# Kernel optimization log

Measured on AMD Instinct MI355X. Metric: run time of the kernel, lower is better.

The kernel has to match this reference:

```python
import jax, jax.numpy as jnp
import numpy as np

B, S, D = 32, 4096, 64
EPS_DIV = 1e-8
EPS_LN = 1e-5  # torch LayerNorm default


def setup_inputs() -> dict:
    key = jax.random.key(0)
    k1, k2, k3 = jax.random.split(key, 3)
    C = jax.random.normal(k1, (B, S, D), dtype=jnp.float32)
    V = jax.random.normal(k2, (B, S, D), dtype=jnp.float32)
    W = jax.random.normal(k3, (B, S, D), dtype=jnp.float32)
    time_mod = jnp.ones((1, 1, D), dtype=jnp.float32) * 0.5  # matches init: ones * 0.5
    ln_gamma = jnp.ones((D,), dtype=jnp.float32)
    ln_beta = jnp.zeros((D,), dtype=jnp.float32)
    return {"C": C, "V": V, "W": W, "time_mod": time_mod,
            "ln_gamma": ln_gamma, "ln_beta": ln_beta}


def reference(C, V, W, time_mod, ln_gamma, ln_beta):
    # Precompute elementwise quantities once (fused, no per-step kernels)
    decay = jax.nn.sigmoid(W * time_mod)        # [B,S,D]
    eC = jnp.exp(C)                             # [B,S,D]

    # scan over sequence axis; move S to the front for lax.scan
    xs = (jnp.swapaxes(decay, 0, 1),            # [S,B,D]
          jnp.swapaxes(eC, 0, 1),
          jnp.swapaxes(V, 0, 1))

    a0 = jnp.zeros((C.shape[0], 1), dtype=C.dtype)
    b0 = jnp.zeros((C.shape[0], C.shape[2]), dtype=C.dtype)

    def step(carry, x):
        a, b = carry
        d, ec, v = x                            # each [B,D]
        a = jnp.mean(d, axis=1, keepdims=True) * a + jnp.sum(ec, axis=1, keepdims=True)
        b = d * b + ec * v
        return (a, b), b / (a + EPS_DIV)

    _, ys = jax.lax.scan(step, (a0, b0), xs)    # ys: [S,B,D]
    result = jnp.swapaxes(ys, 0, 1)             # [B,S,D]

    # LayerNorm over last dim
    mu = jnp.mean(result, axis=-1, keepdims=True)
    var = jnp.var(result, axis=-1, keepdims=True)
    normed = (result - mu) * jax.lax.rsqrt(var + EPS_LN)
    return normed * ln_gamma + ln_beta
```

## Files before the change

### kernel.cpp

```cpp
#include <hip/hip_runtime.h>
#include <hip/hip_fp16.h>

constexpr int B = 32, S = 4096, D = 64;
constexpr float EPS_DIV = 1e-8f;
constexpr float EPS_LN  = 1e-5f;

constexpr int NCG = 1024;
constexpr int LG  = S / NCG;
constexpr int CPL = NCG / 64;
constexpr int BPB = NCG / 16;

struct alignas(16) H2x4 { __half2 a, b, c, d; };

__device__ __forceinline__ float sigmoid_f(float x) {
    return __builtin_amdgcn_rcpf(1.f + __expf(-x));
}

__device__ __forceinline__ void gsum2(float& x, float& y) {
#pragma unroll
    for (int m = 1; m < 16; m <<= 1) {
        x += __shfl_xor(x, m, 64);
        y += __shfl_xor(y, m, 64);
    }
}

__global__ __launch_bounds__(256) void k1h(
    const float4* __restrict__ C4, const float4* __restrict__ V4,
    const float4* __restrict__ W4, const float* __restrict__ TM,
    float2* __restrict__ MQstep,
    float*  __restrict__ Mc, float* __restrict__ Qc,
    float4* __restrict__ Pt4, float4* __restrict__ Ot4,
    H2x4*   __restrict__ dgev)
{
    __shared__ float sp[64][17];
    __shared__ float so[64][17];

    const int t = threadIdx.x;
    const int g = t >> 4;
    const int r = t & 15;
    const int G = blockIdx.x * 16 + g;
    const int b = G >> 10;
    const int c = G & (NCG - 1);
    const int c0 = (blockIdx.x & (BPB - 1)) * 16;
    const int s0 = c * LG;
    const size_t base = (size_t)(b * S + s0) * 16 + r;
    const float4 tm = reinterpret_cast<const float4*>(TM)[r];

    float M = 1.f, Q = 0.f;
    float4 P = {1.f, 1.f, 1.f, 1.f}, O = {0.f, 0.f, 0.f, 0.f};
#pragma unroll
    for (int i = 0; i < LG; ++i) {
        const size_t idx = base + (size_t)i * 16;
        const float4 w = W4[idx], cc = C4[idx], v = V4[idx];
        float4 dg, ec;
        dg.x = sigmoid_f(w.x * tm.x); dg.y = sigmoid_f(w.y * tm.y);
        dg.z = sigmoid_f(w.z * tm.z); dg.w = sigmoid_f(w.w * tm.w);
        ec.x = __expf(cc.x); ec.y = __expf(cc.y);
        ec.z = __expf(cc.z); ec.w = __expf(cc.w);
        float sd = (dg.x + dg.y) + (dg.z + dg.w);
        float se = (ec.x + ec.y) + (ec.z + ec.w);
        gsum2(sd, se);
        const float mm = sd * (1.f / 64.f);
        if (r == 0) MQstep[b * S + s0 + i] = make_float2(mm, se);
        M *= mm;
        Q  = fmaf(mm, Q, se);
        H2x4 hq;
        hq.a = __floats2half2_rn(dg.x, ec.x * v.x);
        hq.b = __floats2half2_rn(dg.y, ec.y * v.y);
        hq.c = __floats2half2_rn(dg.z, ec.z * v.z);
        hq.d = __floats2half2_rn(dg.w, ec.w * v.w);
        dgev[idx] = hq;
        const float2 f0 = __half22float2(hq.a);
        const float2 f1 = __half22float2(hq.b);
        const float2 f2 = __half22float2(hq.c);
        const float2 f3 = __half22float2(hq.d);
        P.x *= f0.x; P.y *= f1.x; P.z *= f2.x; P.w *= f3.x;
        O.x = fmaf(f0.x, O.x, f0.y);
        O.y = fmaf(f1.x, O.y, f1.y);
        O.z = fmaf(f2.x, O.z, f2.y);
        O.w = fmaf(f3.x, O.w, f3.y);
    }
    if (r == 0) { Mc[G] = M; Qc[G] = Q; }

    sp[4*r+0][g] = P.x; sp[4*r+1][g] = P.y; sp[4*r+2][g] = P.z; sp[4*r+3][g] = P.w;
    so[4*r+0][g] = O.x; so[4*r+1][g] = O.y; so[4*r+2][g] = O.z; so[4*r+3][g] = O.w;
    __syncthreads();
    const int d  = t >> 2;
    const int cq = t & 3;
    const float4 vp = make_float4(sp[d][cq*4+0], sp[d][cq*4+1],
                                  sp[d][cq*4+2], sp[d][cq*4+3]);
    const float4 vo = make_float4(so[d][cq*4+0], so[d][cq*4+1],
                                  so[d][cq*4+2], so[d][cq*4+3]);
    const size_t row4 = (size_t)(b * D + d) * (NCG / 4);
    Pt4[row4 + (c0 >> 2) + cq] = vp;
    Ot4[row4 + (c0 >> 2) + cq] = vo;
}

__global__ __launch_bounds__(256) void k2(
    const float*  __restrict__ Mc,  const float*  __restrict__ Qc,
    const float4* __restrict__ Pt4, const float4* __restrict__ Ot4,
    float4* __restrict__ aIn4,
    float4* __restrict__ bIn4)
{
    const int wq   = threadIdx.x >> 6;
    const int lane = threadIdx.x & 63;

    if (blockIdx.x < 512) {
        const int W = blockIdx.x * 4 + wq;
        const int b = W >> 6, d = W & 63;
        const size_t row4 = (size_t)(b * D + d) * (NCG / 4);
        float pj[CPL], oj[CPL];
#pragma unroll
        for (int q4 = 0; q4 < 4; ++q4) {
            const float4 pv = Pt4[row4 + lane*4 + q4];
            const float4 ov = Ot4[row4 + lane*4 + q4];
            pj[q4*4+0] = pv.x; pj[q4*4+1] = pv.y; pj[q4*4+2] = pv.z; pj[q4*4+3] = pv.w;
            oj[q4*4+0] = ov.x; oj[q4*4+1] = ov.y; oj[q4*4+2] = ov.z; oj[q4*4+3] = ov.w;
        }
        float p = 1.f, o = 0.f;
#pragma unroll
        for (int j = 0; j < CPL; ++j) { o = fmaf(pj[j], o, oj[j]); p = pj[j] * p; }
#pragma unroll
        for (int s = 1; s < 64; s <<= 1) {
            const float pp = __shfl_up(p, s, 64);
            const float oo = __shfl_up(o, s, 64);
            if (lane >= s) { o = fmaf(p, oo, o); p = p * pp; }
        }
        float oe = __shfl_up(o, 1, 64);
        if (lane == 0) oe = 0.f;
        float bv = oe;
#pragma unroll
        for (int q4 = 0; q4 < 4; ++q4) {
            float4 w;
            w.x = bv; bv = fmaf(pj[q4*4+0], bv, oj[q4*4+0]);
            w.y = bv; bv = fmaf(pj[q4*4+1], bv, oj[q4*4+1]);
            w.z = bv; bv = fmaf(pj[q4*4+2], bv, oj[q4*4+2]);
            w.w = bv; bv = fmaf(pj[q4*4+3], bv, oj[q4*4+3]);
            bIn4[row4 + lane*4 + q4] = w;
        }
    } else {
        const int v = (blockIdx.x - 512) * 4 + wq;
        if (v >= B) return;
        const float4* Mc4 = reinterpret_cast<const float4*>(Mc) + v * (NCG / 4);
        const float4* Qc4 = reinterpret_cast<const float4*>(Qc) + v * (NCG / 4);
        float mj[CPL], qj[CPL];
#pragma unroll
        for (int q4 = 0; q4 < 4; ++q4) {
            const float4 mv = Mc4[lane*4 + q4];
            const float4 qv = Qc4[lane*4 + q4];
            mj[q4*4+0] = mv.x; mj[q4*4+1] = mv.y; mj[q4*4+2] = mv.z; mj[q4*4+3] = mv.w;
            qj[q4*4+0] = qv.x; qj[q4*4+1] = qv.y; qj[q4*4+2] = qv.z; qj[q4*4+3] = qv.w;
        }
        float m = 1.f, q = 0.f;
#pragma unroll
        for (int j = 0; j < CPL; ++j) { q = fmaf(mj[j], q, qj[j]); m = mj[j] * m; }
#pragma unroll
        for (int s = 1; s < 64; s <<= 1) {
            const float mm = __shfl_up(m, s, 64);
            const float qq = __shfl_up(q, s, 64);
            if (lane >= s) { q = fmaf(m, qq, q); m = m * mm; }
        }
        float qe = __shfl_up(q, 1, 64);
        if (lane == 0) qe = 0.f;
        float a = qe;
        float4* out4 = reinterpret_cast<float4*>(aIn4) + v * (NCG / 4);
#pragma unroll
        for (int q4 = 0; q4 < 4; ++q4) {
            float4 w;
            w.x = a; a = fmaf(mj[q4*4+0], a, qj[q4*4+0]);
            w.y = a; a = fmaf(mj[q4*4+1], a, qj[q4*4+1]);
            w.z = a; a = fmaf(mj[q4*4+2], a, qj[q4*4+2]);
            w.w = a; a = fmaf(mj[q4*4+3], a, qj[q4*4+3]);
            out4[lane*4 + q4] = w;
        }
    }
}

__global__ __launch_bounds__(256) void k3h(
    const H2x4* __restrict__ dgev,
    const float* __restrict__ Gam, const float* __restrict__ Bet,
    const float2* __restrict__ MQstep,
    const float* __restrict__ aIn, const float4* __restrict__ bInT4,
    float4* __restrict__ out4)
{
    __shared__ float sb[64][17];

    const int t = threadIdx.x;
    const int b  = blockIdx.x >> 6;
    const int c0 = (blockIdx.x & (BPB - 1)) * 16;
    {
        const int d = t >> 2, cq = t & 3;
        const float4 ld = bInT4[(size_t)(b * D + d) * (NCG / 4) + (c0 >> 2) + cq];
        sb[d][cq*4+0] = ld.x; sb[d][cq*4+1] = ld.y;
        sb[d][cq*4+2] = ld.z; sb[d][cq*4+3] = ld.w;
    }
    __syncthreads();

    const int g = t >> 4;
    const int r = t & 15;
    const int c = c0 + g;
    const int s0 = c * LG;
    const size_t base = (size_t)(b * S + s0) * 16 + r;
    const float4 g4 = reinterpret_cast<const float4*>(Gam)[r];
    const float4 b4 = reinterpret_cast<const float4*>(Bet)[r];

    float a = aIn[b * NCG + c];
    float4 bv = make_float4(sb[4*r+0][g], sb[4*r+1][g],
                            sb[4*r+2][g], sb[4*r+3][g]);
#pragma unroll
    for (int i = 0; i < LG; ++i) {
        const size_t idx = base + (size_t)i * 16;
        const H2x4 hq = dgev[idx];
        const float2 f0 = __half22float2(hq.a);
        const float2 f1 = __half22float2(hq.b);
        const float2 f2 = __half22float2(hq.c);
        const float2 f3 = __half22float2(hq.d);
        const float2 mq = MQstep[b * S + s0 + i];
        a = fmaf(mq.x, a, mq.y);
        bv.x = fmaf(f0.x, bv.x, f0.y);
        bv.y = fmaf(f1.x, bv.y, f1.y);
        bv.z = fmaf(f2.x, bv.z, f2.y);
        bv.w = fmaf(f3.x, bv.w, f3.y);
        const float inva = __builtin_amdgcn_rcpf(a + EPS_DIV);
        float4 y;
        y.x = bv.x * inva; y.y = bv.y * inva;
        y.z = bv.z * inva; y.w = bv.w * inva;
        float sy = (y.x + y.y) + (y.z + y.w);
        float sq = fmaf(y.x, y.x, y.y * y.y) + fmaf(y.z, y.z, y.w * y.w);
        gsum2(sy, sq);
        const float mu  = sy * (1.f / 64.f);
        const float var = fmaf(-mu, mu, sq * (1.f / 64.f));
        const float rs  = __builtin_amdgcn_rsqf(fmaxf(var, 0.f) + EPS_LN);
        float4 o;
        o.x = fmaf((y.x - mu) * rs, g4.x, b4.x);
        o.y = fmaf((y.y - mu) * rs, g4.y, b4.y);
        o.z = fmaf((y.z - mu) * rs, g4.z, b4.z);
        o.w = fmaf((y.w - mu) * rs, g4.w, b4.w);
        out4[idx] = o;
    }
}

__global__ __launch_bounds__(64) void k_naive(
    const float* __restrict__ Cp, const float* __restrict__ Vp,
    const float* __restrict__ Wp, const float* __restrict__ TM,
    const float* __restrict__ Gam, const float* __restrict__ Bet,
    float* __restrict__ out)
{
    const int b = blockIdx.x;
    const int lane = threadIdx.x;
    const float tm = TM[lane], g = Gam[lane], bt = Bet[lane];
    float a = 0.f, bv = 0.f;
    for (int s = 0; s < S; ++s) {
        const size_t idx = ((size_t)b * S + s) * D + lane;
        const float wv = Wp[idx], cv = Cp[idx], vv = Vp[idx];
        const float dg = sigmoid_f(wv * tm);
        const float ec = __expf(cv);
        float sd = dg, se = ec;
#pragma unroll
        for (int m = 1; m < 64; m <<= 1) {
            sd += __shfl_xor(sd, m, 64);
            se += __shfl_xor(se, m, 64);
        }
        a  = fmaf(sd * (1.f / 64.f), a, se);
        bv = fmaf(dg, bv, ec * vv);
        const float y = bv * __builtin_amdgcn_rcpf(a + EPS_DIV);
        float sy = y, sq = y * y;
#pragma unroll
        for (int m = 1; m < 64; m <<= 1) {
            sy += __shfl_xor(sy, m, 64);
            sq += __shfl_xor(sq, m, 64);
        }
        const float mu  = sy * (1.f / 64.f);
        const float var = fmaf(-mu, mu, sq * (1.f / 64.f));
        const float rs  = __builtin_amdgcn_rsqf(fmaxf(var, 0.f) + EPS_LN);
        out[idx] = fmaf((y - mu) * rs, g, bt);
    }
}

extern "C" void kernel_launch(void* const* d_in, const int* in_sizes, int n_in,
                              void* d_out, int out_size, void* d_ws, size_t ws_size,
                              hipStream_t stream) {
    const float* Cp  = (const float*)d_in[0];
    const float* Vp  = (const float*)d_in[1];
    const float* Wp  = (const float*)d_in[2];
    const float* TM  = (const float*)d_in[3];
    const float* Gam = (const float*)d_in[4];
    const float* Bet = (const float*)d_in[5];
    float* out = (float*)d_out;
    float* wsf = (float*)d_ws;

    const size_t f_mq   = (size_t)B * S * 2;
    const size_t f_scG  = (size_t)B * NCG;
    const size_t f_vecG = (size_t)B * NCG * D;
    const size_t f_base = f_mq + 3 * f_scG + 3 * f_vecG;
    const size_t f_dgev = (size_t)B * S * D;
    const size_t needH  = (f_base + f_dgev) * sizeof(float);

    if (ws_size >= needH) {
        float2* MQstep = (float2*)wsf;
        float* Mc  = wsf + f_mq;
        float* Qc  = Mc + f_scG;
        float* Pt  = Qc + f_scG;
        float* Ot  = Pt + f_vecG;
        float* aIn = Ot + f_vecG;
        float* bIn = aIn + f_scG;
        H2x4* dgev = (H2x4*)(wsf + f_base);

        const dim3 blk(256);
        const dim3 grd(B * NCG / 16);

        k1h<<<grd, blk, 0, stream>>>((const float4*)Cp, (const float4*)Vp,
                                     (const float4*)Wp, TM, MQstep, Mc, Qc,
                                     (float4*)Pt, (float4*)Ot, dgev);
        k2<<<dim3(512 + 8), blk, 0, stream>>>(Mc, Qc, (const float4*)Pt,
                                              (const float4*)Ot,
                                              (float4*)aIn, (float4*)bIn);
        k3h<<<grd, blk, 0, stream>>>(dgev, Gam, Bet, MQstep,
                                     aIn, (const float4*)bIn, (float4*)out);
        return;
    }

    k_naive<<<dim3(B), dim3(64), 0, stream>>>(Cp, Vp, Wp, TM, Gam, Bet, out);
}
```

Before: 49.01 us.

## Halve chunk count, pack chunk P/O summaries as half2, nontemporal output stores

Reduces the number of sequence chunks per batch from 1024 to 512, so each chunk covers 8 steps and the cross-chunk scan works on fewer elements. Chunk decay-product and offset summaries are stored interleaved as half2 pairs instead of two fp32 arrays, which cuts intermediate traffic between the first and second kernels. The final LayerNorm output uses nontemporal stores. Storing the product and offset in half precision risks accuracy loss, especially underflow of the decay products over longer chunks, and each thread in the first and third kernels now does more serial work.

New measurement: 42.05 us. -14.2%, faster.

```diff
diff --git a/kernel.cpp b/kernel.cpp
--- a/kernel.cpp
+++ b/kernel.cpp
@@ -5,12 +5,19 @@
 constexpr float EPS_DIV = 1e-8f;
 constexpr float EPS_LN  = 1e-5f;
 
-constexpr int NCG = 1024;
+constexpr int NCG = 512;
 constexpr int LG  = S / NCG;
 constexpr int CPL = NCG / 64;
 constexpr int BPB = NCG / 16;
 
 struct alignas(16) H2x4 { __half2 a, b, c, d; };
+
+typedef float f4v __attribute__((ext_vector_type(4)));
+
+__device__ __forceinline__ void nt_store_f4(float4 v, float4* p) {
+    f4v t = {v.x, v.y, v.z, v.w};
+    __builtin_nontemporal_store(t, (f4v*)p);
+}
 
 __device__ __forceinline__ float sigmoid_f(float x) {
     return __builtin_amdgcn_rcpf(1.f + __expf(-x));
@@ -29,7 +36,7 @@
     const float4* __restrict__ W4, const float* __restrict__ TM,
     float2* __restrict__ MQstep,
     float*  __restrict__ Mc, float* __restrict__ Qc,
-    float4* __restrict__ Pt4, float4* __restrict__ Ot4,
+    H2x4*   __restrict__ POt,
     H2x4*   __restrict__ dgev)
 {
     __shared__ float sp[64][17];
@@ -39,7 +46,7 @@
     const int g = t >> 4;
     const int r = t & 15;
     const int G = blockIdx.x * 16 + g;
-    const int b = G >> 10;
+    const int b = G >> 9;
     const int c = G & (NCG - 1);
     const int c0 = (blockIdx.x & (BPB - 1)) * 16;
     const int s0 = c * LG;
@@ -87,18 +94,17 @@
     __syncthreads();
     const int d  = t >> 2;
     const int cq = t & 3;
-    const float4 vp = make_float4(sp[d][cq*4+0], sp[d][cq*4+1],
-                                  sp[d][cq*4+2], sp[d][cq*4+3]);
-    const float4 vo = make_float4(so[d][cq*4+0], so[d][cq*4+1],
-                                  so[d][cq*4+2], so[d][cq*4+3]);
-    const size_t row4 = (size_t)(b * D + d) * (NCG / 4);
-    Pt4[row4 + (c0 >> 2) + cq] = vp;
-    Ot4[row4 + (c0 >> 2) + cq] = vo;
+    H2x4 po;
+    po.a = __floats2half2_rn(sp[d][cq*4+0], so[d][cq*4+0]);
+    po.b = __floats2half2_rn(sp[d][cq*4+1], so[d][cq*4+1]);
+    po.c = __floats2half2_rn(sp[d][cq*4+2], so[d][cq*4+2]);
+    po.d = __floats2half2_rn(sp[d][cq*4+3], so[d][cq*4+3]);
+    POt[(size_t)(b * D + d) * (NCG / 4) + (c0 >> 2) + cq] = po;
 }
 
 __global__ __launch_bounds__(256) void k2(
     const float*  __restrict__ Mc,  const float*  __restrict__ Qc,
-    const float4* __restrict__ Pt4, const float4* __restrict__ Ot4,
+    const H2x4*   __restrict__ POt,
     float4* __restrict__ aIn4,
     float4* __restrict__ bIn4)
 {
@@ -109,13 +115,18 @@
         const int W = blockIdx.x * 4 + wq;
         const int b = W >> 6, d = W & 63;
         const size_t row4 = (size_t)(b * D + d) * (NCG / 4);
+        const H2x4 A = POt[row4 + lane*2], Bq = POt[row4 + lane*2 + 1];
         float pj[CPL], oj[CPL];
-#pragma unroll
-        for (int q4 = 0; q4 < 4; ++q4) {
-            const float4 pv = Pt4[row4 + lane*4 + q4];
-            const float4 ov = Ot4[row4 + lane*4 + q4];
-            pj[q4*4+0] = pv.x; pj[q4*4+1] = pv.y; pj[q4*4+2] = pv.z; pj[q4*4+3] = pv.w;
-            oj[q4*4+0] = ov.x; oj[q4*4+1] = ov.y; oj[q4*4+2] = ov.z; oj[q4*4+3] = ov.w;
+        {
+            float2 f;
+            f = __half22float2(A.a);  pj[0] = f.x; oj[0] = f.y;
+            f = __half22float2(A.b);  pj[1] = f.x; oj[1] = f.y;
+            f = __half22float2(A.c);  pj[2] = f.x; oj[2] = f.y;
+            f = __half22float2(A.d);  pj[3] = f.x; oj[3] = f.y;
+            f = __half22float2(Bq.a); pj[4] = f.x; oj[4] = f.y;
+            f = __half22float2(Bq.b); pj[5] = f.x; oj[5] = f.y;
+            f = __half22float2(Bq.c); pj[6] = f.x; oj[6] = f.y;
+            f = __half22float2(Bq.d); pj[7] = f.x; oj[7] = f.y;
         }
         float p = 1.f, o = 0.f;
 #pragma unroll
@@ -128,29 +139,20 @@
         }
         float oe = __shfl_up(o, 1, 64);
         if (lane == 0) oe = 0.f;
-        float bv = oe;
-#pragma unroll
-        for (int q4 = 0; q4 < 4; ++q4) {
-            float4 w;
-            w.x = bv; bv = fmaf(pj[q4*4+0], bv, oj[q4*4+0]);
-            w.y = bv; bv = fmaf(pj[q4*4+1], bv, oj[q4*4+1]);
-            w.z = bv; bv = fmaf(pj[q4*4+2], bv, oj[q4*4+2]);
-            w.w = bv; bv = fmaf(pj[q4*4+3], bv, oj[q4*4+3]);
-            bIn4[row4 + lane*4 + q4] = w;
-        }
+        float bv = oe, ob[CPL];
+#pragma unroll
+        for (int j = 0; j < CPL; ++j) { ob[j] = bv; bv = fmaf(pj[j], bv, oj[j]); }
+        bIn4[row4 + lane*2]     = make_float4(ob[0], ob[1], ob[2], ob[3]);
+        bIn4[row4 + lane*2 + 1] = make_float4(ob[4], ob[5], ob[6], ob[7]);
     } else {
         const int v = (blockIdx.x - 512) * 4 + wq;
         if (v >= B) return;
         const float4* Mc4 = reinterpret_cast<const float4*>(Mc) + v * (NCG / 4);
         const float4* Qc4 = reinterpret_cast<const float4*>(Qc) + v * (NCG / 4);
-        float mj[CPL], qj[CPL];
-#pragma unroll
-        for (int q4 = 0; q4 < 4; ++q4) {
-            const float4 mv = Mc4[lane*4 + q4];
-            const float4 qv = Qc4[lane*4 + q4];
-            mj[q4*4+0] = mv.x; mj[q4*4+1] = mv.y; mj[q4*4+2] = mv.z; mj[q4*4+3] = mv.w;
-            qj[q4*4+0] = qv.x; qj[q4*4+1] = qv.y; qj[q4*4+2] = qv.z; qj[q4*4+3] = qv.w;
-        }
+        const float4 mA = Mc4[lane*2], mB = Mc4[lane*2 + 1];
+        const float4 qA = Qc4[lane*2], qB = Qc4[lane*2 + 1];
+        float mj[CPL] = {mA.x, mA.y, mA.z, mA.w, mB.x, mB.y, mB.z, mB.w};
+        float qj[CPL] = {qA.x, qA.y, qA.z, qA.w, qB.x, qB.y, qB.z, qB.w};
         float m = 1.f, q = 0.f;
 #pragma unroll
         for (int j = 0; j < CPL; ++j) { q = fmaf(mj[j], q, qj[j]); m = mj[j] * m; }
@@ -162,17 +164,11 @@
         }
         float qe = __shfl_up(q, 1, 64);
         if (lane == 0) qe = 0.f;
-        float a = qe;
-        float4* out4 = reinterpret_cast<float4*>(aIn4) + v * (NCG / 4);
-#pragma unroll
-        for (int q4 = 0; q4 < 4; ++q4) {
-            float4 w;
-            w.x = a; a = fmaf(mj[q4*4+0], a, qj[q4*4+0]);
-            w.y = a; a = fmaf(mj[q4*4+1], a, qj[q4*4+1]);
-            w.z = a; a = fmaf(mj[q4*4+2], a, qj[q4*4+2]);
-            w.w = a; a = fmaf(mj[q4*4+3], a, qj[q4*4+3]);
-            out4[lane*4 + q4] = w;
-        }
+        float a = qe, ab[CPL];
+#pragma unroll
+        for (int j = 0; j < CPL; ++j) { ab[j] = a; a = fmaf(mj[j], a, qj[j]); }
+        aIn4[v * (NCG / 4) + lane*2]     = make_float4(ab[0], ab[1], ab[2], ab[3]);
+        aIn4[v * (NCG / 4) + lane*2 + 1] = make_float4(ab[4], ab[5], ab[6], ab[7]);
     }
 }
 
@@ -186,7 +182,7 @@
     __shared__ float sb[64][17];
 
     const int t = threadIdx.x;
-    const int b  = blockIdx.x >> 6;
+    const int b  = blockIdx.x >> 5;
     const int c0 = (blockIdx.x & (BPB - 1)) * 16;
     {
         const int d = t >> 2, cq = t & 3;
@@ -236,7 +232,7 @@
         o.y = fmaf((y.y - mu) * rs, g4.y, b4.y);
         o.z = fmaf((y.z - mu) * rs, g4.z, b4.z);
         o.w = fmaf((y.w - mu) * rs, g4.w, b4.w);
-        out4[idx] = o;
+        nt_store_f4(o, &out4[idx]);
     }
 }
 
@@ -292,28 +288,29 @@
     const size_t f_mq   = (size_t)B * S * 2;
     const size_t f_scG  = (size_t)B * NCG;
     const size_t f_vecG = (size_t)B * NCG * D;
-    const size_t f_base = f_mq + 3 * f_scG + 3 * f_vecG;
+    const size_t f_po   = f_vecG / 2;
+    const size_t f_base = f_mq + 2 * f_scG + f_vecG  + f_scG + f_vecG;
     const size_t f_dgev = (size_t)B * S * D;
     const size_t needH  = (f_base + f_dgev) * sizeof(float);
+    (void)f_po;
 
     if (ws_size >= needH) {
         float2* MQstep = (float2*)wsf;
-        float* Mc  = wsf + f_mq;
-        float* Qc  = Mc + f_scG;
-        float* Pt  = Qc + f_scG;
-        float* Ot  = Pt + f_vecG;
-        float* aIn = Ot + f_vecG;
-        float* bIn = aIn + f_scG;
-        H2x4* dgev = (H2x4*)(wsf + f_base);
+        float* Mc   = wsf + f_mq;
+        float* Qc   = Mc + f_scG;
+        float* POf  = Qc + f_scG;
+        float* aIn  = POf + f_vecG;
+        float* bIn  = aIn + f_scG;
+        H2x4*  dgev = (H2x4*)(wsf + f_base);
+        H2x4*  POt  = (H2x4*)POf;
 
         const dim3 blk(256);
         const dim3 grd(B * NCG / 16);
 
         k1h<<<grd, blk, 0, stream>>>((const float4*)Cp, (const float4*)Vp,
                                      (const float4*)Wp, TM, MQstep, Mc, Qc,
-                                     (float4*)Pt, (float4*)Ot, dgev);
-        k2<<<dim3(512 + 8), blk, 0, stream>>>(Mc, Qc, (const float4*)Pt,
-                                              (const float4*)Ot,
+                                     POt, dgev);
+        k2<<<dim3(512 + 8), blk, 0, stream>>>(Mc, Qc, POt,
                                               (float4*)aIn, (float4*)bIn);
         k3h<<<grd, blk, 0, stream>>>(dgev, Gam, Bet, MQstep,
                                      aIn, (const float4*)bIn, (float4*)out);
```
